# Optimization experiments

Measured on AMD Instinct MI355X. Metric: run time of the kernel, lower is better.

## Reference

```python
import jax, jax.numpy as jnp
import numpy as np

ALPHA = 0.2  # LeakyReLU negative slope


def setup_inputs() -> dict:
    key = jax.random.key(0)
    k1, k2, k3, k4 = jax.random.split(key, 4)
    N, E, F_IN, F_OUT = 100000, 1600000, 128, 32
    x = jax.random.normal(k1, (N, F_IN), dtype=jnp.float32)
    W = jax.random.normal(k2, (F_IN, F_OUT), dtype=jnp.float32) * 0.1
    a = jax.random.normal(k3, (2 * F_OUT, 1), dtype=jnp.float32) * 0.1
    edge_index = jax.random.randint(k4, (2, E), 0, N, dtype=jnp.int64)
    return {"x": x, "W": W, "a": a, "edge_index": edge_index}


def reference(x, W, a, edge_index):
    N = x.shape[0]
    F_OUT = W.shape[1]
    Wx = x @ W  # [N, F_OUT]
    src = edge_index[0]  # row indices (softmax groups)
    dst = edge_index[1]
    # e = leakyrelu([Wx_i || Wx_j] @ a); split a to avoid materializing the concat
    a_src = a[:F_OUT, 0]
    a_dst = a[F_OUT:, 0]
    e = (Wx @ a_src)[src] + (Wx @ a_dst)[dst]  # [E]
    e = jnp.where(e >= 0, e, ALPHA * e)
    # sparse softmax over rows (src)
    m = jax.ops.segment_max(e, src, num_segments=N)  # -inf for empty rows
    m = jnp.where(jnp.isinf(m), 0.0, m)
    exp_v = jnp.exp(e - m[src])
    s = jax.ops.segment_sum(exp_v, src, num_segments=N)
    s = jnp.where(s == 0, 1.0, s)
    att = exp_v / s[src]  # [E]
    # sparse matmul: h[i] = sum_j att[i,j] * Wx[j]
    h = jax.ops.segment_sum(att[:, None] * Wx[dst], src, num_segments=N)
    return jax.nn.elu(h)
```

## Files before the change

kernel.cpp:

```cpp
#include <hip/hip_runtime.h>
#include <hip/hip_bf16.h>
#include <math.h>

#define ALPHA 0.2f
#define F_IN 128
#define F_OUT 32
#define BSHIFT 7
#define BNODES 128
#define DSTBITS 17
#define CHUNK 2048
#define SLABCAP 3072
#define NBKMAX 800
#define MAXPER 12

typedef __attribute__((ext_vector_type(8))) short short8;
typedef __attribute__((ext_vector_type(4))) float float4v;

__device__ __forceinline__ short f2bf(float f) {
    __hip_bfloat16 h = __float2bfloat16(f);
    return __builtin_bit_cast(short, h);
}
__device__ __forceinline__ float bf2f(unsigned short u) {
    return __uint_as_float((unsigned)u << 16);
}

__global__ __launch_bounds__(256) void k_phaseA(
    const float* __restrict__ x, const float* __restrict__ W,
    const float* __restrict__ a, unsigned short* __restrict__ Wxh,
    float* __restrict__ s1, float* __restrict__ s2, int nTiles, int N, int nT1,
    const int* __restrict__ src, const int* __restrict__ dst,
    int* __restrict__ bcur, unsigned* __restrict__ packed, int E, int NBK)
{
    if ((int)blockIdx.x < nT1) {
        __shared__ short Wt[32 * 136];
        for (int i = threadIdx.x; i < F_IN * F_OUT; i += 256) {
            int k = i >> 5, n = i & 31;
            Wt[n * 136 + k] = f2bf(W[i]);
        }
        __syncthreads();

        int wave = threadIdx.x >> 6;
        int lane = threadIdx.x & 63;
        int tile = blockIdx.x * 4 + wave;
        if (tile >= nTiles) return;

        int m    = lane & 15;
        int quad = lane >> 4;
        int row  = tile * 16 + m;
        int rowc = row < N ? row : N - 1;

        short8 bf[2][4];
#pragma unroll
        for (int t = 0; t < 2; ++t)
#pragma unroll
            for (int s = 0; s < 4; ++s)
                bf[t][s] = *(const short8*)&Wt[(t * 16 + m) * 136 + s * 32 + quad * 8];

        float4v acc0 = {0.f, 0.f, 0.f, 0.f};
        float4v acc1 = {0.f, 0.f, 0.f, 0.f};
        const float* xr = x + (size_t)rowc * F_IN + quad * 8;
#pragma unroll
        for (int s = 0; s < 4; ++s) {
            float4 xa = *(const float4*)(xr + s * 32);
            float4 xb = *(const float4*)(xr + s * 32 + 4);
            short8 af;
            af[0] = f2bf(xa.x); af[1] = f2bf(xa.y); af[2] = f2bf(xa.z); af[3] = f2bf(xa.w);
            af[4] = f2bf(xb.x); af[5] = f2bf(xb.y); af[6] = f2bf(xb.z); af[7] = f2bf(xb.w);
            acc0 = __builtin_amdgcn_mfma_f32_16x16x32_bf16(af, bf[0][s], acc0, 0, 0, 0);
            acc1 = __builtin_amdgcn_mfma_f32_16x16x32_bf16(af, bf[1][s], acc1, 0, 0, 0);
        }

        int rbase = tile * 16 + quad * 4;
#pragma unroll
        for (int r = 0; r < 4; ++r) {
            if (rbase + r < N) {
                Wxh[(size_t)(rbase + r) * F_OUT + m]      = (unsigned short)f2bf(acc0[r]);
                Wxh[(size_t)(rbase + r) * F_OUT + m + 16] = (unsigned short)f2bf(acc1[r]);
            }
        }

        float a1c0 = a[m], a1c1 = a[m + 16];
        float a2c0 = a[F_OUT + m], a2c1 = a[F_OUT + m + 16];
#pragma unroll
        for (int r = 0; r < 4; ++r) {
            float v1 = acc0[r] * a1c0 + acc1[r] * a1c1;
            float v2 = acc0[r] * a2c0 + acc1[r] * a2c1;
#pragma unroll
            for (int off = 8; off >= 1; off >>= 1) {
                v1 += __shfl_xor(v1, off, 16);
                v2 += __shfl_xor(v2, off, 16);
            }
            if (m == 0 && rbase + r < N) {
                s1[rbase + r] = v1;
                s2[rbase + r] = v2;
            }
        }
    } else {
        __shared__ int hist[NBKMAX];
        __shared__ int cur[NBKMAX];
        int t = threadIdx.x;
        for (int i = t; i < NBK; i += 256) hist[i] = 0;
        __syncthreads();
        int e0 = ((int)blockIdx.x - nT1) * CHUNK;
        int sreg[8], dreg[8];
#pragma unroll
        for (int k = 0; k < 2; ++k) {
            int e = e0 + k * 1024 + t * 4;
            int4 s4, d4;
            if (e + 3 < E) {
                s4 = *(const int4*)&src[e];
                d4 = *(const int4*)&dst[e];
            } else {
                s4.x = (e + 0 < E) ? src[e + 0] : -1;
                s4.y = (e + 1 < E) ? src[e + 1] : -1;
                s4.z = (e + 2 < E) ? src[e + 2] : -1;
                s4.w = (e + 3 < E) ? src[e + 3] : -1;
                d4.x = (e + 0 < E) ? dst[e + 0] : 0;
                d4.y = (e + 1 < E) ? dst[e + 1] : 0;
                d4.z = (e + 2 < E) ? dst[e + 2] : 0;
                d4.w = (e + 3 < E) ? dst[e + 3] : 0;
            }
            sreg[k * 4 + 0] = s4.x; dreg[k * 4 + 0] = d4.x;
            sreg[k * 4 + 1] = s4.y; dreg[k * 4 + 1] = d4.y;
            sreg[k * 4 + 2] = s4.z; dreg[k * 4 + 2] = d4.z;
            sreg[k * 4 + 3] = s4.w; dreg[k * 4 + 3] = d4.w;
        }
#pragma unroll
        for (int k = 0; k < 8; ++k)
            if (sreg[k] >= 0) atomicAdd(&hist[sreg[k] >> BSHIFT], 1);
        __syncthreads();
        for (int i = t; i < NBK; i += 256)
            if (hist[i] > 0) cur[i] = atomicAdd(&bcur[i], hist[i]);
        __syncthreads();
#pragma unroll
        for (int k = 0; k < 8; ++k) {
            if (sreg[k] >= 0) {
                int b = sreg[k] >> BSHIFT;
                int p = atomicAdd(&cur[b], 1);
                if (p < SLABCAP)
                    packed[(size_t)b * SLABCAP + p] =
                        ((unsigned)(sreg[k] & (BNODES - 1)) << DSTBITS) | (unsigned)dreg[k];
            }
        }
    }
}

__global__ __launch_bounds__(256) void k_bnode(
    const unsigned* __restrict__ packed, const int* __restrict__ bcnt,
    const float* __restrict__ s1, const float* __restrict__ s2,
    const unsigned short* __restrict__ Wxh, float* __restrict__ out, int N)
{
    __shared__ unsigned sorted[SLABCAP];
    __shared__ int psum[256];
    __shared__ int rpl[BNODES];
    __shared__ int degl[BNODES];
    __shared__ int cur[BNODES];
    __shared__ int histl[BNODES];
    __shared__ float s1l[BNODES];

    int b = blockIdx.x;
    int t = threadIdx.x;
    int n0 = b << BSHIFT;
    int cnt = min(bcnt[b], SLABCAP);
    const unsigned* pb = packed + (size_t)b * SLABCAP;

    if (t < BNODES) {
        histl[t] = 0;
        int n = n0 + t;
        s1l[t] = (n < N) ? s1[n] : 0.f;
    }
    __syncthreads();

    unsigned ereg[MAXPER];
#pragma unroll
    for (int k = 0; k < MAXPER; ++k) {
        int j = k * 256 + t;
        ereg[k] = (j < cnt) ? pb[j] : 0xFFFFFFFFu;
    }
#pragma unroll
    for (int k = 0; k < MAXPER; ++k)
        if (ereg[k] != 0xFFFFFFFFu) atomicAdd(&histl[ereg[k] >> DSTBITS], 1);
    __syncthreads();

    int a0 = (t < BNODES) ? histl[t] : 0;
    psum[t] = a0;
    __syncthreads();
    for (int off = 1; off < BNODES; off <<= 1) {
        int v = (t >= off) ? psum[t - off] : 0;
        __syncthreads();
        psum[t] += v;
        __syncthreads();
    }
    if (t < BNODES) {
        int excl = (t > 0) ? psum[t - 1] : 0;
        rpl[t] = excl;
        cur[t] = excl;
        degl[t] = a0;
    }
    __syncthreads();

#pragma unroll
    for (int k = 0; k < MAXPER; ++k) {
        if (ereg[k] != 0xFFFFFFFFu) {
            int ls = ereg[k] >> DSTBITS;
            int p = atomicAdd(&cur[ls], 1);
            sorted[p] = ereg[k];
        }
    }
    __syncthreads();

    int g = t >> 5;
    int l = t & 31;
    int es = l >> 3;
    int fl = l & 7;

    for (int ni = 0; ni < BNODES / 8; ++ni) {
        int ls = g * (BNODES / 8) + ni;
        int n = n0 + ls;
        if (n >= N) break;
        int base = rpl[ls];
        int deg  = degl[ls];
        float s1n = s1l[ls];

        float4 acc = {0.f, 0.f, 0.f, 0.f};
        float sum = 0.f;
        for (int j0 = 0; j0 < deg; j0 += 32) {
            int j = j0 + l;
            int   d_l = 0;
            float p_l = 0.f;
            if (j < deg) {
                d_l = (int)(sorted[base + j] & ((1u << DSTBITS) - 1));
                float ev = s1n + s2[d_l];
                ev = ev >= 0.f ? ev : ALPHA * ev;
                p_l = expf(ev);
            }
            sum += p_l;
            int cnt2 = min(32, deg - j0);
            int nIter = (cnt2 + 3) >> 2;
            for (int it = 0; it < nIter; ++it) {
                int e = it * 4 + es;
                float p = __shfl(p_l, e, 32);
                int   d = __shfl(d_l, e, 32);
                ushort4 w = *(const ushort4*)&Wxh[(size_t)d * F_OUT + fl * 4];
                acc.x += p * bf2f(w.x);
                acc.y += p * bf2f(w.y);
                acc.z += p * bf2f(w.z);
                acc.w += p * bf2f(w.w);
            }
        }
#pragma unroll
        for (int off = 8; off <= 16; off <<= 1) {
            acc.x += __shfl_xor(acc.x, off, 32);
            acc.y += __shfl_xor(acc.y, off, 32);
            acc.z += __shfl_xor(acc.z, off, 32);
            acc.w += __shfl_xor(acc.w, off, 32);
        }
#pragma unroll
        for (int off = 16; off >= 1; off >>= 1)
            sum += __shfl_xor(sum, off, 32);

        if (es == 0) {
            float inv = (deg > 0) ? 1.f / sum : 0.f;
            float4 h;
            h.x = acc.x * inv; h.y = acc.y * inv; h.z = acc.z * inv; h.w = acc.w * inv;
            h.x = h.x > 0.f ? h.x : expm1f(h.x);
            h.y = h.y > 0.f ? h.y : expm1f(h.y);
            h.z = h.z > 0.f ? h.z : expm1f(h.z);
            h.w = h.w > 0.f ? h.w : expm1f(h.w);
            *(float4*)&out[(size_t)n * F_OUT + fl * 4] = h;
        }
    }
}

extern "C" void kernel_launch(void* const* d_in, const int* in_sizes, int n_in,
                              void* d_out, int out_size, void* d_ws, size_t ws_size,
                              hipStream_t stream)
{
    const float* x = (const float*)d_in[0];
    const float* W = (const float*)d_in[1];
    const float* a = (const float*)d_in[2];
    const int*  ei = (const int*)d_in[3];

    int N = in_sizes[0] / F_IN;
    int E = in_sizes[3] / 2;
    const int* src = ei;
    const int* dst = ei + E;
    int NBK = (N + BNODES - 1) >> BSHIFT;
    int nTiles = (N + 15) / 16;
    int nT1 = (nTiles + 3) / 4;
    int nEB = (E + CHUNK - 1) / CHUNK;

    unsigned short* Wxh = (unsigned short*)d_ws;
    float*    s1       = (float*)d_ws + (size_t)16 * N;
    float*    s2       = s1 + N;
    int*      bcur     = (int*)(s2 + N);
    unsigned* packed   = (unsigned*)(bcur + NBKMAX);

    float* out = (float*)d_out;

    hipMemsetAsync(bcur, 0, (size_t)NBK * 4, stream);

    k_phaseA<<<nT1 + nEB, 256, 0, stream>>>(x, W, a, Wxh, s1, s2, nTiles, N, nT1,
                                            src, dst, bcur, packed, E, NBK);
    k_bnode<<<NBK, 256, 0, stream>>>(packed, bcur, s1, s2, Wxh, out, N);
}
```

Baseline: 180.3 us.

## Widen blocks to 512 threads, pad bucket counters, vectorize neighbor gathers

Doubles block size for both kernels and quadruples the edge chunk per binning block, which cuts the number of global atomics on bucket counters. Pads each bucket counter to its own 64-byte slot to reduce contention between counters. In the aggregation kernel each lane now loads 8 bf16 features (16 bytes) per neighbor, so 8 edges are processed in parallel per 32-lane group, and fast __expf replaces expf. The trade-offs are higher register pressure, fewer blocks in flight for the node-bucket kernel, and slightly lower exp accuracy.

```diff
diff --git a/kernel.cpp b/kernel.cpp
--- a/kernel.cpp
+++ b/kernel.cpp
@@ -8,10 +8,11 @@
 #define BSHIFT 7
 #define BNODES 128
 #define DSTBITS 17
-#define CHUNK 2048
+#define CHUNK 8192
 #define SLABCAP 3072
 #define NBKMAX 800
-#define MAXPER 12
+#define MAXPER 6
+#define CURSTRIDE 16
 
 typedef __attribute__((ext_vector_type(8))) short short8;
 typedef __attribute__((ext_vector_type(4))) float float4v;
@@ -20,11 +21,14 @@
     __hip_bfloat16 h = __float2bfloat16(f);
     return __builtin_bit_cast(short, h);
 }
-__device__ __forceinline__ float bf2f(unsigned short u) {
-    return __uint_as_float((unsigned)u << 16);
-}
-
-__global__ __launch_bounds__(256) void k_phaseA(
+__device__ __forceinline__ float bf_lo(unsigned u) {
+    return __uint_as_float(u << 16);
+}
+__device__ __forceinline__ float bf_hi(unsigned u) {
+    return __uint_as_float(u & 0xFFFF0000u);
+}
+
+__global__ __launch_bounds__(512) void k_phaseA(
     const float* __restrict__ x, const float* __restrict__ W,
     const float* __restrict__ a, unsigned short* __restrict__ Wxh,
     float* __restrict__ s1, float* __restrict__ s2, int nTiles, int N, int nT1,
@@ -33,7 +37,7 @@
 {
     if ((int)blockIdx.x < nT1) {
         __shared__ short Wt[32 * 136];
-        for (int i = threadIdx.x; i < F_IN * F_OUT; i += 256) {
+        for (int i = threadIdx.x; i < F_IN * F_OUT; i += 512) {
             int k = i >> 5, n = i & 31;
             Wt[n * 136 + k] = f2bf(W[i]);
         }
@@ -41,7 +45,7 @@
 
         int wave = threadIdx.x >> 6;
         int lane = threadIdx.x & 63;
-        int tile = blockIdx.x * 4 + wave;
+        int tile = blockIdx.x * 8 + wave;
         if (tile >= nTiles) return;
 
         int m    = lane & 15;
@@ -99,13 +103,13 @@
         __shared__ int hist[NBKMAX];
         __shared__ int cur[NBKMAX];
         int t = threadIdx.x;
-        for (int i = t; i < NBK; i += 256) hist[i] = 0;
+        for (int i = t; i < NBK; i += 512) hist[i] = 0;
         __syncthreads();
         int e0 = ((int)blockIdx.x - nT1) * CHUNK;
-        int sreg[8], dreg[8];
-#pragma unroll
-        for (int k = 0; k < 2; ++k) {
-            int e = e0 + k * 1024 + t * 4;
+        int sreg[16], dreg[16];
+#pragma unroll
+        for (int k = 0; k < 4; ++k) {
+            int e = e0 + k * 2048 + t * 4;
             int4 s4, d4;
             if (e + 3 < E) {
                 s4 = *(const int4*)&src[e];
@@ -126,14 +130,14 @@
             sreg[k * 4 + 3] = s4.w; dreg[k * 4 + 3] = d4.w;
         }
 #pragma unroll
-        for (int k = 0; k < 8; ++k)
+        for (int k = 0; k < 16; ++k)
             if (sreg[k] >= 0) atomicAdd(&hist[sreg[k] >> BSHIFT], 1);
         __syncthreads();
-        for (int i = t; i < NBK; i += 256)
-            if (hist[i] > 0) cur[i] = atomicAdd(&bcur[i], hist[i]);
-        __syncthreads();
-#pragma unroll
-        for (int k = 0; k < 8; ++k) {
+        for (int i = t; i < NBK; i += 512)
+            if (hist[i] > 0) cur[i] = atomicAdd(&bcur[i * CURSTRIDE], hist[i]);
+        __syncthreads();
+#pragma unroll
+        for (int k = 0; k < 16; ++k) {
             if (sreg[k] >= 0) {
                 int b = sreg[k] >> BSHIFT;
                 int p = atomicAdd(&cur[b], 1);
@@ -145,13 +149,13 @@
     }
 }
 
-__global__ __launch_bounds__(256) void k_bnode(
-    const unsigned* __restrict__ packed, const int* __restrict__ bcnt,
+__global__ __launch_bounds__(512) void k_bnode(
+    const unsigned* __restrict__ packed, const int* __restrict__ bcur,
     const float* __restrict__ s1, const float* __restrict__ s2,
     const unsigned short* __restrict__ Wxh, float* __restrict__ out, int N)
 {
     __shared__ unsigned sorted[SLABCAP];
-    __shared__ int psum[256];
+    __shared__ int psum[BNODES];
     __shared__ int rpl[BNODES];
     __shared__ int degl[BNODES];
     __shared__ int cur[BNODES];
@@ -161,7 +165,7 @@
     int b = blockIdx.x;
     int t = threadIdx.x;
     int n0 = b << BSHIFT;
-    int cnt = min(bcnt[b], SLABCAP);
+    int cnt = min(bcur[b * CURSTRIDE], SLABCAP);
     const unsigned* pb = packed + (size_t)b * SLABCAP;
 
     if (t < BNODES) {
@@ -174,7 +178,7 @@
     unsigned ereg[MAXPER];
 #pragma unroll
     for (int k = 0; k < MAXPER; ++k) {
-        int j = k * 256 + t;
+        int j = k * 512 + t;
         ereg[k] = (j < cnt) ? pb[j] : 0xFFFFFFFFu;
     }
 #pragma unroll
@@ -182,13 +186,14 @@
         if (ereg[k] != 0xFFFFFFFFu) atomicAdd(&histl[ereg[k] >> DSTBITS], 1);
     __syncthreads();
 
-    int a0 = (t < BNODES) ? histl[t] : 0;
-    psum[t] = a0;
+    int a0 = 0;
+    if (t < BNODES) { a0 = histl[t]; psum[t] = a0; }
     __syncthreads();
     for (int off = 1; off < BNODES; off <<= 1) {
-        int v = (t >= off) ? psum[t - off] : 0;
-        __syncthreads();
-        psum[t] += v;
+        int v = 0;
+        if (t < BNODES && t >= off) v = psum[t - off];
+        __syncthreads();
+        if (t < BNODES) psum[t] += v;
         __syncthreads();
     }
     if (t < BNODES) {
@@ -211,19 +216,22 @@
 
     int g = t >> 5;
     int l = t & 31;
-    int es = l >> 3;
-    int fl = l & 7;
-
-    for (int ni = 0; ni < BNODES / 8; ++ni) {
-        int ls = g * (BNODES / 8) + ni;
+    int es = l >> 2;
+    int fq = l & 3;
+
+    for (int ni = 0; ni < 8; ++ni) {
+        int ls = g * 8 + ni;
         int n = n0 + ls;
         if (n >= N) break;
         int base = rpl[ls];
         int deg  = degl[ls];
         float s1n = s1l[ls];
 
-        float4 acc = {0.f, 0.f, 0.f, 0.f};
+        float acc[8];
+#pragma unroll
+        for (int c = 0; c < 8; ++c) acc[c] = 0.f;
         float sum = 0.f;
+
         for (int j0 = 0; j0 < deg; j0 += 32) {
             int j = j0 + l;
             int   d_l = 0;
@@ -232,42 +240,51 @@
                 d_l = (int)(sorted[base + j] & ((1u << DSTBITS) - 1));
                 float ev = s1n + s2[d_l];
                 ev = ev >= 0.f ? ev : ALPHA * ev;
-                p_l = expf(ev);
+                p_l = __expf(ev);
             }
             sum += p_l;
             int cnt2 = min(32, deg - j0);
-            int nIter = (cnt2 + 3) >> 2;
+            int nIter = (cnt2 + 7) >> 3;
             for (int it = 0; it < nIter; ++it) {
-                int e = it * 4 + es;
+                int e = it * 8 + es;
                 float p = __shfl(p_l, e, 32);
                 int   d = __shfl(d_l, e, 32);
-                ushort4 w = *(const ushort4*)&Wxh[(size_t)d * F_OUT + fl * 4];
-                acc.x += p * bf2f(w.x);
-                acc.y += p * bf2f(w.y);
-                acc.z += p * bf2f(w.z);
-                acc.w += p * bf2f(w.w);
-            }
-        }
-#pragma unroll
-        for (int off = 8; off <= 16; off <<= 1) {
-            acc.x += __shfl_xor(acc.x, off, 32);
-            acc.y += __shfl_xor(acc.y, off, 32);
-            acc.z += __shfl_xor(acc.z, off, 32);
-            acc.w += __shfl_xor(acc.w, off, 32);
-        }
+                uint4 w = *(const uint4*)&Wxh[(size_t)d * F_OUT + fq * 8];
+                acc[0] += p * bf_lo(w.x);
+                acc[1] += p * bf_hi(w.x);
+                acc[2] += p * bf_lo(w.y);
+                acc[3] += p * bf_hi(w.y);
+                acc[4] += p * bf_lo(w.z);
+                acc[5] += p * bf_hi(w.z);
+                acc[6] += p * bf_lo(w.w);
+                acc[7] += p * bf_hi(w.w);
+            }
+        }
+#pragma unroll
+        for (int off = 4; off <= 16; off <<= 1)
+#pragma unroll
+            for (int c = 0; c < 8; ++c)
+                acc[c] += __shfl_xor(acc[c], off, 32);
 #pragma unroll
         for (int off = 16; off >= 1; off >>= 1)
             sum += __shfl_xor(sum, off, 32);
 
         if (es == 0) {
             float inv = (deg > 0) ? 1.f / sum : 0.f;
-            float4 h;
-            h.x = acc.x * inv; h.y = acc.y * inv; h.z = acc.z * inv; h.w = acc.w * inv;
-            h.x = h.x > 0.f ? h.x : expm1f(h.x);
-            h.y = h.y > 0.f ? h.y : expm1f(h.y);
-            h.z = h.z > 0.f ? h.z : expm1f(h.z);
-            h.w = h.w > 0.f ? h.w : expm1f(h.w);
-            *(float4*)&out[(size_t)n * F_OUT + fl * 4] = h;
+            float4 h0, h1;
+            h0.x = acc[0] * inv; h0.y = acc[1] * inv; h0.z = acc[2] * inv; h0.w = acc[3] * inv;
+            h1.x = acc[4] * inv; h1.y = acc[5] * inv; h1.z = acc[6] * inv; h1.w = acc[7] * inv;
+            h0.x = h0.x > 0.f ? h0.x : expm1f(h0.x);
+            h0.y = h0.y > 0.f ? h0.y : expm1f(h0.y);
+            h0.z = h0.z > 0.f ? h0.z : expm1f(h0.z);
+            h0.w = h0.w > 0.f ? h0.w : expm1f(h0.w);
+            h1.x = h1.x > 0.f ? h1.x : expm1f(h1.x);
+            h1.y = h1.y > 0.f ? h1.y : expm1f(h1.y);
+            h1.z = h1.z > 0.f ? h1.z : expm1f(h1.z);
+            h1.w = h1.w > 0.f ? h1.w : expm1f(h1.w);
+            float* op = &out[(size_t)n * F_OUT + fq * 8];
+            *(float4*)op       = h0;
+            *(float4*)(op + 4) = h1;
         }
     }
 }
@@ -287,20 +304,20 @@
     const int* dst = ei + E;
     int NBK = (N + BNODES - 1) >> BSHIFT;
     int nTiles = (N + 15) / 16;
-    int nT1 = (nTiles + 3) / 4;
+    int nT1 = (nTiles + 7) / 8;
     int nEB = (E + CHUNK - 1) / CHUNK;
 
     unsigned short* Wxh = (unsigned short*)d_ws;
     float*    s1       = (float*)d_ws + (size_t)16 * N;
     float*    s2       = s1 + N;
     int*      bcur     = (int*)(s2 + N);
-    unsigned* packed   = (unsigned*)(bcur + NBKMAX);
+    unsigned* packed   = (unsigned*)(bcur + NBKMAX * CURSTRIDE);
 
     float* out = (float*)d_out;
 
-    hipMemsetAsync(bcur, 0, (size_t)NBK * 4, stream);
-
-    k_phaseA<<<nT1 + nEB, 256, 0, stream>>>(x, W, a, Wxh, s1, s2, nTiles, N, nT1,
+    hipMemsetAsync(bcur, 0, (size_t)NBKMAX * CURSTRIDE * 4, stream);
+
+    k_phaseA<<<nT1 + nEB, 512, 0, stream>>>(x, W, a, Wxh, s1, s2, nTiles, N, nT1,
                                             src, dst, bcur, packed, E, NBK);
-    k_bnode<<<NBK, 256, 0, stream>>>(packed, bcur, s1, s2, Wxh, out, N);
-}
+    k_bnode<<<NBK, 512, 0, stream>>>(packed, bcur, s1, s2, Wxh, out, N);
+}
```

New measurement: 156.6 us. 1.15x faster.
